# Optimization experiments

Hardware: AMD Instinct MI355X
Metric: run time of the kernel (lower is better)

The kernel has to match this reference:

```python
import jax, jax.numpy as jnp
import numpy as np

N_NODES = 50000
N_EDGES = 1_600_000
FEAT, HIDDEN, NUM_CLASS = 128, 128, 64


def setup_inputs() -> dict:
    key = jax.random.key(0)
    k1, k2, k3, k4, k5 = jax.random.split(key, 5)
    h = jax.random.normal(k1, (N_NODES, FEAT), dtype=jnp.float32)
    edge_index = jax.random.randint(k2, (2, N_EDGES), 0, N_NODES, dtype=jnp.int32)
    # Glorot-ish init for the three GraphConv weights (bias=False)
    W1 = jax.random.normal(k3, (FEAT, HIDDEN), dtype=jnp.float32) * (1.0 / np.sqrt(FEAT))
    W2 = jax.random.normal(k4, (HIDDEN, HIDDEN), dtype=jnp.float32) * (1.0 / np.sqrt(HIDDEN))
    W3 = jax.random.normal(k5, (HIDDEN, NUM_CLASS), dtype=jnp.float32) * (1.0 / np.sqrt(HIDDEN))
    return {"h": h, "edge_index": edge_index, "W1": W1, "W2": W2, "W3": W3}


def _gcn_layer(h, W, src, dst, out_isqrt, in_isqrt, n_nodes):
    # DGL GraphConv, norm='both', bias=False: relu( D_in^{-1/2} A D_out^{-1/2} h W )
    h = h * out_isqrt[:, None]          # scale source features
    h = h @ W                            # dense projection (order-invariant)
    agg = jax.ops.segment_sum(h[src], dst, num_segments=n_nodes)  # SpMM aggregation
    agg = agg * in_isqrt[:, None]
    return jax.nn.relu(agg)


def reference(h, edge_index, W1, W2, W3):
    src, dst = edge_index[0], edge_index[1]
    ones = jnp.ones(src.shape[0], dtype=h.dtype)
    out_deg = jax.ops.segment_sum(ones, src, num_segments=N_NODES)
    in_deg = jax.ops.segment_sum(ones, dst, num_segments=N_NODES)
    out_isqrt = jnp.clip(out_deg, 1.0, None) ** -0.5
    in_isqrt = jnp.clip(in_deg, 1.0, None) ** -0.5
    h = _gcn_layer(h, W1, src, dst, out_isqrt, in_isqrt, N_NODES)
    h = _gcn_layer(h, W2, src, dst, out_isqrt, in_isqrt, N_NODES)
    h = _gcn_layer(h, W3, src, dst, out_isqrt, in_isqrt, N_NODES)
    return h
```

## Files before the change

kernel.cpp:

```cpp
#include <hip/hip_runtime.h>

#define N_NODES 50000
#define N_EDGES 1600000
#define FEAT 128
#define HIDDEN 128
#define NUM_CLASS 64

#define NBUCK 782
#define EPB 2048
#define NBLK 782
#define SCAP 2560
#define AGG_NBN 3125
#define GEMM_BLOCKS 782
#define NSHW 6256

typedef _Float16 h8 __attribute__((ext_vector_type(8)));
typedef _Float16 h4 __attribute__((ext_vector_type(4)));
typedef float f32x4 __attribute__((ext_vector_type(4)));

__global__ __launch_bounds__(256) void passA_kernel(const int* __restrict__ ei,
                                                    unsigned* __restrict__ priv,
                                                    int* __restrict__ localoff,
                                                    int* __restrict__ Cmat,
                                                    unsigned* __restrict__ nibshad,
                                                    const float* __restrict__ W1,
                                                    const float* __restrict__ W2,
                                                    const float* __restrict__ W3,
                                                    _Float16* __restrict__ WhT) {
    const int t = threadIdx.x;
    const int blk = blockIdx.x;
    if (blk >= NBLK) {
        const int id = (blk - NBLK) * 256 + t;
        if (id < 16384) {
            const int n = id >> 7, k = id & 127;
            WhT[id] = (_Float16)W1[k * 128 + n];
        } else if (id < 32768) {
            const int i = id - 16384, n = i >> 7, k = i & 127;
            WhT[id] = (_Float16)W2[k * 128 + n];
        } else if (id < 40960) {
            const int i = id - 32768, n = i >> 7, k = i & 127;
            WhT[id] = (_Float16)W3[k * 64 + n];
        }
        return;
    }
    __shared__ int cnt[1024];
    __shared__ int base[1024];
    __shared__ int cur[1024];
    __shared__ int tmp[256];
    __shared__ unsigned sorted[EPB];
    __shared__ unsigned nib[NSHW];
    for (int i = t; i < 1024; i += 256) cnt[i] = 0;
    for (int i = t; i < NSHW; i += 256) nib[i] = 0;
    __syncthreads();

    const int ebase = blk * EPB;
    unsigned packed[8];
    int bk[8];
#pragma unroll
    for (int j = 0; j < 8; ++j) {
        const int e = ebase + t + j * 256;
        if (e < N_EDGES) {
            const unsigned s = (unsigned)ei[e];
            const unsigned d = (unsigned)ei[N_EDGES + e];
            bk[j] = (int)(d >> 6);
            packed[j] = s | ((d & 63u) << 16) | ((d >> 6) << 22);
            atomicAdd(&cnt[bk[j]], 1);
            atomicAdd(&nib[s >> 3], 1u << ((s & 7u) * 4u));
        } else bk[j] = -1;
    }
    __syncthreads();

    const int c0 = cnt[4*t], c1 = cnt[4*t+1], c2 = cnt[4*t+2], c3 = cnt[4*t+3];
    const int s = c0 + c1 + c2 + c3;
    tmp[t] = s;
    __syncthreads();
    for (int off = 1; off < 256; off <<= 1) {
        int v = (t >= off) ? tmp[t - off] : 0;
        __syncthreads();
        tmp[t] += v;
        __syncthreads();
    }
    const int excl = tmp[t] - s;
    base[4*t] = excl;            cur[4*t] = excl;
    base[4*t+1] = excl+c0;       cur[4*t+1] = excl+c0;
    base[4*t+2] = excl+c0+c1;    cur[4*t+2] = excl+c0+c1;
    base[4*t+3] = excl+c0+c1+c2; cur[4*t+3] = excl+c0+c1+c2;
    __syncthreads();

    for (int b = t; b < NBUCK; b += 256) {
        localoff[(size_t)blk * NBUCK + b] = base[b];
        Cmat[(size_t)blk * NBUCK + b] = cnt[b];
    }
#pragma unroll
    for (int j = 0; j < 8; ++j)
        if (bk[j] >= 0) {
            const int pos = atomicAdd(&cur[bk[j]], 1);
            sorted[pos] = packed[j];
        }
    __syncthreads();
    const int total = min(EPB, N_EDGES - ebase);
    for (int i = t; i < total; i += 256) priv[(size_t)blk * EPB + i] = sorted[i];
    unsigned* dst = nibshad + (size_t)blk * NSHW;
    for (int i = t; i < NSHW; i += 256) dst[i] = nib[i];
}

__global__ __launch_bounds__(256) void setup_kernel(const int* __restrict__ Cmat,
                                                    int* __restrict__ total,
                                                    const unsigned* __restrict__ nibshad,
                                                    float* __restrict__ out_isqrt) {
    const int bid = blockIdx.x;
    const int t = threadIdx.x;
    if (bid < 196) {
        const int b0 = bid * 4;
        const int c = t & 3, r = t >> 2;
        int s = 0;
        if (b0 + c < NBUCK)
            for (int i = r; i < NBLK; i += 64) s += Cmat[(size_t)i * NBUCK + b0 + c];
        __shared__ int red[256];
        red[t] = s;
        __syncthreads();
        for (int off = 128; off >= 4; off >>= 1) {
            if (t < off) red[t] += red[t + off];
            __syncthreads();
        }
        if (t < 4 && b0 + t < NBUCK) total[b0 + t] = red[t];
        return;
    }
    const int blk = bid - 196;
    const int w0 = blk * 8;
    const int wl = t & 7, c = t >> 3;
    int acc[8] = {0, 0, 0, 0, 0, 0, 0, 0};
    for (int sh = c; sh < NBLK; sh += 32) {
        const unsigned u = nibshad[(size_t)sh * NSHW + w0 + wl];
        acc[0] += u & 15u;         acc[1] += (u >> 4) & 15u;
        acc[2] += (u >> 8) & 15u;  acc[3] += (u >> 12) & 15u;
        acc[4] += (u >> 16) & 15u; acc[5] += (u >> 20) & 15u;
        acc[6] += (u >> 24) & 15u; acc[7] += (u >> 28);
    }
    __shared__ int red2[32][8][8];
#pragma unroll
    for (int nb = 0; nb < 8; ++nb) red2[c][wl][nb] = acc[nb];
    __syncthreads();
    for (int off = 16; off > 0; off >>= 1) {
        if (c < off) {
#pragma unroll
            for (int nb = 0; nb < 8; ++nb) red2[c][wl][nb] += red2[c + off][wl][nb];
        }
        __syncthreads();
    }
    if (t < 64) {
        const int wl2 = t >> 3, nb = t & 7;
        const int node = (w0 + wl2) * 8 + nb;
        if (node < N_NODES) {
            const int d = red2[0][wl2][nb];
            out_isqrt[node] = rsqrtf((float)(d < 1 ? 1 : d));
        }
    }
}

template <int OUT, typename InT>
__device__ __forceinline__ void gemm_body(const InT* __restrict__ H,
                                          const _Float16* __restrict__ WhT,
                                          const float* __restrict__ out_isqrt,
                                          _Float16* __restrict__ Ys,
                                          const int bidx, const int tid,
                                          _Float16* Hs) {
    constexpr int NT = OUT / 16;
    char* hb = (char*)Hs;
    const int bn = bidx * 64;

    {
        const int n = tid & 63, kg = tid >> 6;
        const int gn = bn + n;
        const int swz = (n & 7) << 4;
        if (gn < N_NODES) {
            if constexpr (sizeof(InT) == 4) {
                const float4* hrow = (const float4*)(H + (size_t)gn * FEAT) + kg * 8;
#pragma unroll
                for (int jj = 0; jj < 4; ++jj) {
                    const float4 u = hrow[jj * 2];
                    const float4 v = hrow[jj * 2 + 1];
                    h8 r;
                    r[0] = (_Float16)u.x; r[1] = (_Float16)u.y; r[2] = (_Float16)u.z; r[3] = (_Float16)u.w;
                    r[4] = (_Float16)v.x; r[5] = (_Float16)v.y; r[6] = (_Float16)v.z; r[7] = (_Float16)v.w;
                    *(h8*)(hb + ((n * 256 + kg * 64 + jj * 16) ^ swz)) = r;
                }
            } else {
                const h8* hrow = (const h8*)(H + (size_t)gn * FEAT) + kg * 4;
#pragma unroll
                for (int jj = 0; jj < 4; ++jj)
                    *(h8*)(hb + ((n * 256 + kg * 64 + jj * 16) ^ swz)) = hrow[jj];
            }
        } else {
            h8 z;
#pragma unroll
            for (int i = 0; i < 8; ++i) z[i] = (_Float16)0.f;
#pragma unroll
            for (int jj = 0; jj < 4; ++jj)
                *(h8*)(hb + ((n * 256 + kg * 64 + jj * 16) ^ swz)) = z;
        }
    }
    __syncthreads();

    const int l = tid & 63, w = tid >> 6;
    const int lm = l & 15, lk = l >> 4;
    const int nloc = w * 16 + lm;
    const int swzr = (nloc & 7) << 4;

    h8 bfrag[4];
#pragma unroll
    for (int kt = 0; kt < 4; ++kt)
        bfrag[kt] = *(const h8*)(hb + ((nloc * 256 + (lk * 8 + kt * 32) * 2) ^ swzr));

    f32x4 acc[NT];
#pragma unroll
    for (int nt = 0; nt < NT; ++nt) acc[nt] = (f32x4){0.f, 0.f, 0.f, 0.f};

#pragma unroll
    for (int nt = 0; nt < NT; ++nt) {
        const _Float16* wp = WhT + (size_t)(nt * 16 + lm) * 128 + lk * 8;
#pragma unroll
        for (int kt = 0; kt < 4; ++kt) {
            const h8 afrag = *(const h8*)(wp + kt * 32);
            acc[nt] = __builtin_amdgcn_mfma_f32_16x16x32_f16(afrag, bfrag[kt], acc[nt], 0, 0, 0);
        }
    }

    const int node = bn + w * 16 + lm;
    if (node < N_NODES) {
        const float sc = out_isqrt[node];
#pragma unroll
        for (int nt = 0; nt < NT; ++nt) {
            const int f0 = nt * 16 + lk * 4;
            h4 r;
            r[0] = (_Float16)(acc[nt][0] * sc);
            r[1] = (_Float16)(acc[nt][1] * sc);
            r[2] = (_Float16)(acc[nt][2] * sc);
            r[3] = (_Float16)(acc[nt][3] * sc);
            *(h4*)(Ys + ((size_t)(f0 >> 5) * N_NODES + node) * 32 + (f0 & 31)) = r;
        }
    }
}

template <int OUT, typename InT>
__global__ __launch_bounds__(256) void gemm_kernel(const InT* __restrict__ H,
                                                   const _Float16* __restrict__ WhT,
                                                   const float* __restrict__ out_isqrt,
                                                   _Float16* __restrict__ Ys) {
    __shared__ _Float16 Hs[64 * 128];
    gemm_body<OUT, InT>(H, WhT, out_isqrt, Ys, blockIdx.x, threadIdx.x, Hs);
}

__global__ __launch_bounds__(256) void csr2gemm_kernel(const int* __restrict__ localoff,
                                                       const unsigned* __restrict__ priv,
                                                       const int* __restrict__ total,
                                                       unsigned short* __restrict__ csr,
                                                       int* __restrict__ row_off,
                                                       float* __restrict__ in_isqrt,
                                                       const float* __restrict__ H,
                                                       const _Float16* __restrict__ WhT,
                                                       const float* __restrict__ out_isqrt,
                                                       _Float16* __restrict__ Ys) {
    __shared__ char smem[16384];
    const int bid = blockIdx.x;
    const int t = threadIdx.x;
    if (bid >= NBUCK) {
        gemm_body<HIDDEN, float>(H, WhT, out_isqrt, Ys, bid - NBUCK, t, (_Float16*)smem);
        return;
    }
    int* tmp = (int*)smem;
    unsigned* gath = (unsigned*)(smem + 1024);
    int* cnt64 = (int*)(smem + 1024 + SCAP * 4);
    int* cur64 = cnt64 + 64;
    const int b = bid;

    {
        const int g = 4 * t;
        const int s0 = (g < NBUCK) ? total[g] : 0;
        const int s1 = (g + 1 < NBUCK) ? total[g + 1] : 0;
        const int s2 = (g + 2 < NBUCK) ? total[g + 2] : 0;
        const int s3 = (g + 3 < NBUCK) ? total[g + 3] : 0;
        const int s = s0 + s1 + s2 + s3;
        tmp[t] = s;
        __syncthreads();
        for (int off = 1; off < 256; off <<= 1) {
            int v = (t >= off) ? tmp[t - off] : 0;
            __syncthreads();
            tmp[t] += v;
            __syncthreads();
        }
        const int excl = tmp[t] - s;
        __syncthreads();
        tmp[t] = excl;
        __syncthreads();
    }
    int cb = tmp[b >> 2];
    for (int u = (b & ~3); u < b; ++u) cb += total[u];
    __syncthreads();

    int off_[4], len_[4];
#pragma unroll
    for (int u = 0; u < 4; ++u) {
        const int blk = 4 * t + u;
        if (blk < NBLK) {
            const int o = localoff[(size_t)blk * NBUCK + b];
            const int nxt = (b == NBUCK - 1) ? min(EPB, N_EDGES - blk * EPB)
                                             : localoff[(size_t)blk * NBUCK + b + 1];
            off_[u] = o; len_[u] = nxt - o;
        } else { off_[u] = 0; len_[u] = 0; }
    }
    const int s = len_[0] + len_[1] + len_[2] + len_[3];
    tmp[t] = s;
    __syncthreads();
    for (int off = 1; off < 256; off <<= 1) {
        int v = (t >= off) ? tmp[t - off] : 0;
        __syncthreads();
        tmp[t] += v;
        __syncthreads();
    }
    int run = tmp[t] - s;
    const int totalE = tmp[255];
#pragma unroll
    for (int u = 0; u < 4; ++u) {
        const int blk = 4 * t + u;
        const unsigned* srcp = priv + (size_t)blk * EPB + off_[u];
        for (int j = 0; j < len_[u]; ++j)
            if (run + j < SCAP) gath[run + j] = srcp[j];
        run += len_[u];
    }
    if (t < 64) cnt64[t] = 0;
    __syncthreads();

    const int gtot = min(totalE, SCAP);
    for (int i = t; i < gtot; i += 256) atomicAdd(&cnt64[(gath[i] >> 16) & 63u], 1);
    __syncthreads();

    const int v64 = (t < 64) ? cnt64[t] : 0;
    tmp[t] = v64;
    __syncthreads();
    for (int off = 1; off < 64; off <<= 1) {
        int v = (t >= off) ? tmp[t - off] : 0;
        __syncthreads();
        tmp[t] += v;
        __syncthreads();
    }
    if (t < 64) {
        const int myoff = cb + tmp[t] - v64;
        cur64[t] = myoff;
        const int node = b * 64 + t;
        if (node < N_NODES) {
            row_off[node] = myoff;
            in_isqrt[node] = rsqrtf((float)(v64 > 0 ? v64 : 1));
        }
    }
    if (bid == 0 && t == 0) row_off[N_NODES] = N_EDGES;
    __syncthreads();

    for (int i = t; i < gtot; i += 256) {
        const unsigned w = gath[i];
        const int pos = atomicAdd(&cur64[(w >> 16) & 63u], 1);
        csr[pos] = (unsigned short)(w & 0xFFFFu);
    }
}

template <int F, typename OT>
__global__ __launch_bounds__(256) void agg_kernel(const int* __restrict__ row_off,
                                                  const unsigned short* __restrict__ csr,
                                                  const _Float16* __restrict__ Ys,
                                                  const float* __restrict__ in_isqrt,
                                                  OT* __restrict__ out) {
    constexpr int NS = F / 32;
    const int s  = blockIdx.x & (NS - 1);
    const int nb = blockIdx.x / NS;
    const int tid = threadIdx.x;
    const int lane = tid & 63;
    const int j = lane >> 4;
    const int esub = (lane >> 2) & 3;
    const int q = lane & 3;

    const int d = nb * 16 + (tid >> 6) * 4 + j;
    const _Float16* Yp = Ys + (size_t)s * (N_NODES * 32) + q * 8;

    const int end = row_off[d + 1];
    float a0 = 0.f, a1 = 0.f, a2 = 0.f, a3 = 0.f, a4 = 0.f, a5 = 0.f, a6 = 0.f, a7 = 0.f;

    int e = row_off[d] + esub;
    for (; e + 12 < end; e += 16) {
        const int i0 = csr[e];
        const int i1 = csr[e + 4];
        const int i2 = csr[e + 8];
        const int i3 = csr[e + 12];
        const h8 v0 = *(const h8*)(Yp + (size_t)i0 * 32);
        const h8 v1 = *(const h8*)(Yp + (size_t)i1 * 32);
        const h8 v2 = *(const h8*)(Yp + (size_t)i2 * 32);
        const h8 v3 = *(const h8*)(Yp + (size_t)i3 * 32);
        const h8 tsum = (v0 + v1) + (v2 + v3);
        a0 += (float)tsum[0]; a1 += (float)tsum[1];
        a2 += (float)tsum[2]; a3 += (float)tsum[3];
        a4 += (float)tsum[4]; a5 += (float)tsum[5];
        a6 += (float)tsum[6]; a7 += (float)tsum[7];
    }
    for (; e + 4 < end; e += 8) {
        const int i0 = csr[e];
        const int i1 = csr[e + 4];
        const h8 v0 = *(const h8*)(Yp + (size_t)i0 * 32);
        const h8 v1 = *(const h8*)(Yp + (size_t)i1 * 32);
        const h8 tsum = v0 + v1;
        a0 += (float)tsum[0]; a1 += (float)tsum[1];
        a2 += (float)tsum[2]; a3 += (float)tsum[3];
        a4 += (float)tsum[4]; a5 += (float)tsum[5];
        a6 += (float)tsum[6]; a7 += (float)tsum[7];
    }
    if (e < end) {
        const int i0 = csr[e];
        const h8 v0 = *(const h8*)(Yp + (size_t)i0 * 32);
        a0 += (float)v0[0]; a1 += (float)v0[1]; a2 += (float)v0[2]; a3 += (float)v0[3];
        a4 += (float)v0[4]; a5 += (float)v0[5]; a6 += (float)v0[6]; a7 += (float)v0[7];
    }

    a0 += __shfl_xor(a0, 4, 64); a0 += __shfl_xor(a0, 8, 64);
    a1 += __shfl_xor(a1, 4, 64); a1 += __shfl_xor(a1, 8, 64);
    a2 += __shfl_xor(a2, 4, 64); a2 += __shfl_xor(a2, 8, 64);
    a3 += __shfl_xor(a3, 4, 64); a3 += __shfl_xor(a3, 8, 64);
    a4 += __shfl_xor(a4, 4, 64); a4 += __shfl_xor(a4, 8, 64);
    a5 += __shfl_xor(a5, 4, 64); a5 += __shfl_xor(a5, 8, 64);
    a6 += __shfl_xor(a6, 4, 64); a6 += __shfl_xor(a6, 8, 64);
    a7 += __shfl_xor(a7, 4, 64); a7 += __shfl_xor(a7, 8, 64);

    if (esub == 0) {
        const float isq = in_isqrt[d];
        const float r0 = fmaxf(a0 * isq, 0.f), r1 = fmaxf(a1 * isq, 0.f);
        const float r2 = fmaxf(a2 * isq, 0.f), r3 = fmaxf(a3 * isq, 0.f);
        const float r4 = fmaxf(a4 * isq, 0.f), r5 = fmaxf(a5 * isq, 0.f);
        const float r6 = fmaxf(a6 * isq, 0.f), r7 = fmaxf(a7 * isq, 0.f);
        if constexpr (sizeof(OT) == 2) {
            h8 o;
            o[0] = (_Float16)r0; o[1] = (_Float16)r1; o[2] = (_Float16)r2; o[3] = (_Float16)r3;
            o[4] = (_Float16)r4; o[5] = (_Float16)r5; o[6] = (_Float16)r6; o[7] = (_Float16)r7;
            *(h8*)((_Float16*)out + (size_t)d * F + s * 32 + q * 8) = o;
        } else {
            float* op = (float*)out + (size_t)d * F + s * 32 + q * 8;
            float4 w0 = {r0, r1, r2, r3}, w1 = {r4, r5, r6, r7};
            *(float4*)op = w0;
            *(float4*)(op + 4) = w1;
        }
    }
}

extern "C" void kernel_launch(void* const* d_in, const int* in_sizes, int n_in,
                              void* d_out, int out_size, void* d_ws, size_t ws_size,
                              hipStream_t stream) {
    const float* h  = (const float*)d_in[0];
    const int*   ei = (const int*)d_in[1];
    const float* W1 = (const float*)d_in[2];
    const float* W2 = (const float*)d_in[3];
    const float* W3 = (const float*)d_in[4];
    float* out = (float*)d_out;

    char* p = (char*)d_ws;
    auto alloc = [&p](size_t bytes) {
        void* r = (void*)p;
        p += (bytes + 255) & ~(size_t)255;
        return r;
    };
    int*   row_off  = (int*)alloc((N_NODES + 1) * sizeof(int));
    int*   total    = (int*)alloc(NBUCK * sizeof(int));
    unsigned short* csr = (unsigned short*)alloc((size_t)N_EDGES * sizeof(unsigned short));
    float* in_isqrt  = (float*)alloc(N_NODES * sizeof(float));
    float* out_isqrt = (float*)alloc(N_NODES * sizeof(float));
    _Float16* WhT   = (_Float16*)alloc(40960 * sizeof(_Float16));
    _Float16* Ys    = (_Float16*)alloc((size_t)N_NODES * HIDDEN * sizeof(_Float16));
    _Float16* bufA  = (_Float16*)alloc((size_t)N_NODES * HIDDEN * sizeof(_Float16));
    _Float16* bufB  = (_Float16*)alloc((size_t)N_NODES * HIDDEN * sizeof(_Float16));
    unsigned* nibshad = (unsigned*)alloc((size_t)NBLK * NSHW * sizeof(unsigned));
    unsigned* priv   = (unsigned*)bufA;
    int* localoff    = (int*)bufB;
    int* Cmat        = localoff + (size_t)NBLK * NBUCK;

    passA_kernel<<<NBLK + 160, 256, 0, stream>>>(ei, priv, localoff, Cmat, nibshad,
                                                 W1, W2, W3, WhT);
    setup_kernel<<<978, 256, 0, stream>>>(Cmat, total, nibshad, out_isqrt);
    csr2gemm_kernel<<<NBUCK + GEMM_BLOCKS, 256, 0, stream>>>(localoff, priv, total,
                                                             csr, row_off, in_isqrt,
                                                             h, WhT, out_isqrt, Ys);

    agg_kernel<HIDDEN, _Float16><<<4 * AGG_NBN, 256, 0, stream>>>(row_off, csr, Ys, in_isqrt, bufA);

    gemm_kernel<HIDDEN, _Float16><<<GEMM_BLOCKS, 256, 0, stream>>>(bufA, WhT + 16384, out_isqrt, Ys);
    agg_kernel<HIDDEN, _Float16><<<4 * AGG_NBN, 256, 0, stream>>>(row_off, csr, Ys, in_isqrt, bufB);

    gemm_kernel<NUM_CLASS, _Float16><<<GEMM_BLOCKS, 256, 0, stream>>>(bufB, WhT + 32768, out_isqrt, Ys);
    agg_kernel<NUM_CLASS, float><<<2 * AGG_NBN, 256, 0, stream>>>(row_off, csr, Ys, in_isqrt, out);
}
```

Baseline: 216.1 us.

## Group four destination buckets per block in CSR build phase

The CSR construction blocks now each handle four 64-node buckets (256 nodes) instead of one, so there are about a quarter as many CSR blocks. Each block reads a contiguous range of localoff per source block and gathers larger runs from priv into a bigger shared buffer. The per-bucket global prefix scan over totals is replaced by a reduction over preceding buckets, followed by a 256-wide local scan. The aim is fewer, longer contiguous reads and less repeated prefix work, at the cost of larger shared memory per block (lower occupancy) and less parallelism in the CSR phase.

```diff
diff --git a/kernel.cpp b/kernel.cpp
--- a/kernel.cpp
+++ b/kernel.cpp
@@ -9,7 +9,8 @@
 #define NBUCK 782
 #define EPB 2048
 #define NBLK 782
-#define SCAP 2560
+#define NGRP 196
+#define GCAP 8704
 #define AGG_NBN 3125
 #define GEMM_BLOCKS 782
 #define NSHW 6256
@@ -261,55 +262,35 @@
                                                        const _Float16* __restrict__ WhT,
                                                        const float* __restrict__ out_isqrt,
                                                        _Float16* __restrict__ Ys) {
-    __shared__ char smem[16384];
+    __shared__ char smem[GCAP * 4 + 3 * 1024];
     const int bid = blockIdx.x;
     const int t = threadIdx.x;
-    if (bid >= NBUCK) {
-        gemm_body<HIDDEN, float>(H, WhT, out_isqrt, Ys, bid - NBUCK, t, (_Float16*)smem);
+    if (bid >= NGRP) {
+        gemm_body<HIDDEN, float>(H, WhT, out_isqrt, Ys, bid - NGRP, t, (_Float16*)smem);
         return;
     }
-    int* tmp = (int*)smem;
-    unsigned* gath = (unsigned*)(smem + 1024);
-    int* cnt64 = (int*)(smem + 1024 + SCAP * 4);
-    int* cur64 = cnt64 + 64;
-    const int b = bid;
-
-    {
-        const int g = 4 * t;
-        const int s0 = (g < NBUCK) ? total[g] : 0;
-        const int s1 = (g + 1 < NBUCK) ? total[g + 1] : 0;
-        const int s2 = (g + 2 < NBUCK) ? total[g + 2] : 0;
-        const int s3 = (g + 3 < NBUCK) ? total[g + 3] : 0;
-        const int s = s0 + s1 + s2 + s3;
-        tmp[t] = s;
-        __syncthreads();
-        for (int off = 1; off < 256; off <<= 1) {
-            int v = (t >= off) ? tmp[t - off] : 0;
-            __syncthreads();
-            tmp[t] += v;
-            __syncthreads();
-        }
-        const int excl = tmp[t] - s;
-        __syncthreads();
-        tmp[t] = excl;
-        __syncthreads();
-    }
-    int cb = tmp[b >> 2];
-    for (int u = (b & ~3); u < b; ++u) cb += total[u];
-    __syncthreads();
-
-    int off_[4], len_[4];
+    unsigned* gath = (unsigned*)smem;
+    int* tmp    = (int*)(smem + GCAP * 4);
+    int* cnt256 = tmp + 256;
+    int* cur256 = cnt256 + 256;
+
+    const int g = bid;
+    const int b0 = 4 * g;
+    const int nb = (NBUCK - b0 < 4) ? (NBUCK - b0) : 4;
+    const int nnode = nb * 64;
+
+    int st_[4], ln_[4];
 #pragma unroll
     for (int u = 0; u < 4; ++u) {
         const int blk = 4 * t + u;
         if (blk < NBLK) {
-            const int o = localoff[(size_t)blk * NBUCK + b];
-            const int nxt = (b == NBUCK - 1) ? min(EPB, N_EDGES - blk * EPB)
-                                             : localoff[(size_t)blk * NBUCK + b + 1];
-            off_[u] = o; len_[u] = nxt - o;
-        } else { off_[u] = 0; len_[u] = 0; }
-    }
-    const int s = len_[0] + len_[1] + len_[2] + len_[3];
+            const int st = localoff[(size_t)blk * NBUCK + b0];
+            const int en = (b0 + nb < NBUCK) ? localoff[(size_t)blk * NBUCK + b0 + nb]
+                                             : min(EPB, N_EDGES - blk * EPB);
+            st_[u] = st; ln_[u] = en - st;
+        } else { st_[u] = 0; ln_[u] = 0; }
+    }
+    const int s = ln_[0] + ln_[1] + ln_[2] + ln_[3];
     tmp[t] = s;
     __syncthreads();
     for (int off = 1; off < 256; off <<= 1) {
@@ -318,47 +299,65 @@
         tmp[t] += v;
         __syncthreads();
     }
+    const int gtot0 = tmp[255];
     int run = tmp[t] - s;
-    const int totalE = tmp[255];
 #pragma unroll
     for (int u = 0; u < 4; ++u) {
         const int blk = 4 * t + u;
-        const unsigned* srcp = priv + (size_t)blk * EPB + off_[u];
-        for (int j = 0; j < len_[u]; ++j)
-            if (run + j < SCAP) gath[run + j] = srcp[j];
-        run += len_[u];
-    }
-    if (t < 64) cnt64[t] = 0;
-    __syncthreads();
-
-    const int gtot = min(totalE, SCAP);
-    for (int i = t; i < gtot; i += 256) atomicAdd(&cnt64[(gath[i] >> 16) & 63u], 1);
-    __syncthreads();
-
-    const int v64 = (t < 64) ? cnt64[t] : 0;
-    tmp[t] = v64;
-    __syncthreads();
-    for (int off = 1; off < 64; off <<= 1) {
-        int v = (t >= off) ? tmp[t - off] : 0;
-        __syncthreads();
-        tmp[t] += v;
-        __syncthreads();
-    }
-    if (t < 64) {
-        const int myoff = cb + tmp[t] - v64;
-        cur64[t] = myoff;
-        const int node = b * 64 + t;
+        const unsigned* srcp = priv + (size_t)blk * EPB + st_[u];
+        for (int j = 0; j < ln_[u]; ++j)
+            if (run + j < GCAP) gath[run + j] = srcp[j];
+        run += ln_[u];
+    }
+    cnt256[t] = 0;
+    __syncthreads();
+
+    const int gtot = min(gtot0, GCAP);
+    for (int i = t; i < gtot; i += 256) {
+        const unsigned w = gath[i];
+        const int nid = (int)((w >> 22) - (unsigned)b0) * 64 + (int)((w >> 16) & 63u);
+        atomicAdd(&cnt256[nid], 1);
+    }
+    __syncthreads();
+
+    {
+        int sb = 0;
+        for (int b = t; b < b0; b += 256) sb += total[b];
+        tmp[t] = sb;
+        __syncthreads();
+        for (int off = 128; off > 0; off >>= 1) {
+            if (t < off) tmp[t] += tmp[t + off];
+            __syncthreads();
+        }
+    }
+    const int base_g = tmp[0];
+    __syncthreads();
+
+    const int v = cnt256[t];
+    tmp[t] = v;
+    __syncthreads();
+    for (int off = 1; off < 256; off <<= 1) {
+        int x = (t >= off) ? tmp[t - off] : 0;
+        __syncthreads();
+        tmp[t] += x;
+        __syncthreads();
+    }
+    const int myoff = base_g + tmp[t] - v;
+    cur256[t] = myoff;
+    if (t < nnode) {
+        const int node = g * 256 + t;
         if (node < N_NODES) {
             row_off[node] = myoff;
-            in_isqrt[node] = rsqrtf((float)(v64 > 0 ? v64 : 1));
-        }
-    }
-    if (bid == 0 && t == 0) row_off[N_NODES] = N_EDGES;
+            in_isqrt[node] = rsqrtf((float)(v > 0 ? v : 1));
+        }
+    }
+    if (g == 0 && t == 0) row_off[N_NODES] = N_EDGES;
     __syncthreads();
 
     for (int i = t; i < gtot; i += 256) {
         const unsigned w = gath[i];
-        const int pos = atomicAdd(&cur64[(w >> 16) & 63u], 1);
+        const int nid = (int)((w >> 22) - (unsigned)b0) * 64 + (int)((w >> 16) & 63u);
+        const int pos = atomicAdd(&cur256[nid], 1);
         csr[pos] = (unsigned short)(w & 0xFFFFu);
     }
 }
@@ -480,9 +479,9 @@
     passA_kernel<<<NBLK + 160, 256, 0, stream>>>(ei, priv, localoff, Cmat, nibshad,
                                                  W1, W2, W3, WhT);
     setup_kernel<<<978, 256, 0, stream>>>(Cmat, total, nibshad, out_isqrt);
-    csr2gemm_kernel<<<NBUCK + GEMM_BLOCKS, 256, 0, stream>>>(localoff, priv, total,
-                                                             csr, row_off, in_isqrt,
-                                                             h, WhT, out_isqrt, Ys);
+    csr2gemm_kernel<<<NGRP + GEMM_BLOCKS, 256, 0, stream>>>(localoff, priv, total,
+                                                            csr, row_off, in_isqrt,
+                                                            h, WhT, out_isqrt, Ys);
 
     agg_kernel<HIDDEN, _Float16><<<4 * AGG_NBN, 256, 0, stream>>>(row_off, csr, Ys, in_isqrt, bufA);
 
```

After: 227.5 us. 5.3% more time.
